# Performance work log

Hardware: AMD Instinct MI355X
Metric: run time of the kernel (lower is better)

## Reference

```python
import jax, jax.numpy as jnp
import numpy as np

D = 128   # latent_dim
H = 128   # mlp_hidden_dim
S = 2     # message_passing_steps
NM = 30000   # mesh nodes
NO = 2000    # obj nodes
EMM = 240000 # mesh->mesh edges
EMO = 60000  # mesh->obj edges


def _ln(h, g, b):
    m = jnp.mean(h, axis=-1, keepdims=True)
    v = jnp.mean((h - m) ** 2, axis=-1, keepdims=True)
    return (h - m) * jax.lax.rsqrt(v + 1e-5) * g + b


def _mlp_ln(h, W0, b0, W1, b1, W2, b2, g, bt):
    # build_mlp(in, [H]*2, out) + LayerNorm(out)
    h = jax.nn.relu(h @ W0 + b0)
    h = jax.nn.relu(h @ W1 + b1)
    h = h @ W2 + b2
    return _ln(h, g, bt)


def _edge_conv(x_src, x_dst, ei, ea, W0, b0, W1, b1, W2, b2, g, bt):
    # PyG source_to_target: x_j = src gather (ei[0]), x_i = dst gather (ei[1])
    xi = x_dst[ei[1]]
    xj = x_src[ei[0]]
    msg = _mlp_ln(jnp.concatenate([xi, xj, ea], axis=-1), W0, b0, W1, b1, W2, b2, g, bt)
    aggr = jax.ops.segment_sum(msg, ei[1], num_segments=x_dst.shape[0])
    return ea + msg, aggr  # residual on edge attr; aggr is sum of raw messages


def _node_conv(x, aggr, W0, b0, W1, b1, W2, b2, g, bt):
    return x + _mlp_ln(jnp.concatenate([x, aggr], axis=-1), W0, b0, W1, b1, W2, b2, g, bt)


def setup_inputs() -> dict:
    key = jax.random.key(0)
    ks = jax.random.split(key, 16)
    f = jnp.float32
    x_mesh = jax.random.normal(ks[0], (NM, D), f)
    x_obj = jax.random.normal(ks[1], (NO, D), f)
    ea_mm = jax.random.normal(ks[2], (EMM, D), f)
    ea_mo = jax.random.normal(ks[3], (EMO, D), f)
    ei_mm = jnp.stack([jax.random.randint(ks[4], (EMM,), 0, NM),
                       jax.random.randint(ks[5], (EMM,), 0, NM)]).astype(jnp.int32)
    ei_mo = jnp.stack([jax.random.randint(ks[6], (EMO,), 0, NM),
                       jax.random.randint(ks[7], (EMO,), 0, NO)]).astype(jnp.int32)

    def w(k, shape, fan):
        return jax.random.normal(k, shape, f) * (1.0 / np.sqrt(fan))

    # params stacked as [edge_or_node_type(2), step(S), ...]
    eW0 = w(ks[8], (2, S, 3 * D, H), 3 * D); eb0 = jnp.zeros((2, S, H), f)
    eW1 = w(ks[9], (2, S, H, H), H);         eb1 = jnp.zeros((2, S, H), f)
    eW2 = w(ks[10], (2, S, H, D), H);        eb2 = jnp.zeros((2, S, D), f)
    eg = jnp.ones((2, S, D), f);             ebt = jnp.zeros((2, S, D), f)
    nW0 = w(ks[11], (2, S, 2 * D, H), 2 * D); nb0 = jnp.zeros((2, S, H), f)
    nW1 = w(ks[12], (2, S, H, H), H);         nb1 = jnp.zeros((2, S, H), f)
    nW2 = w(ks[13], (2, S, H, D), H);         nb2 = jnp.zeros((2, S, D), f)
    ng = jnp.ones((2, S, D), f);              nbt = jnp.zeros((2, S, D), f)
    return dict(x_mesh=x_mesh, x_obj=x_obj, ei_mm=ei_mm, ei_mo=ei_mo,
                ea_mm=ea_mm, ea_mo=ea_mo,
                eW0=eW0, eb0=eb0, eW1=eW1, eb1=eb1, eW2=eW2, eb2=eb2, eg=eg, ebt=ebt,
                nW0=nW0, nb0=nb0, nW1=nW1, nb1=nb1, nW2=nW2, nb2=nb2, ng=ng, nbt=nbt)


def reference(x_mesh, x_obj, ei_mm, ei_mo, ea_mm, ea_mo,
              eW0, eb0, eW1, eb1, eW2, eb2, eg, ebt,
              nW0, nb0, nW1, nb1, nW2, nb2, ng, nbt):
    for s in range(S):
        ep = lambda t: (eW0[t, s], eb0[t, s], eW1[t, s], eb1[t, s], eW2[t, s], eb2[t, s], eg[t, s], ebt[t, s])
        npar = lambda t: (nW0[t, s], nb0[t, s], nW1[t, s], nb1[t, s], nW2[t, s], nb2[t, s], ng[t, s], nbt[t, s])
        # edge convs use node features at layer input
        ea_mm, agg_mesh = _edge_conv(x_mesh, x_mesh, ei_mm, ea_mm, *ep(0))
        ea_mo, agg_obj = _edge_conv(x_mesh, x_obj, ei_mo, ea_mo, *ep(1))
        x_mesh = _node_conv(x_mesh, agg_mesh, *npar(0))
        x_obj = _node_conv(x_obj, agg_obj, *npar(1))
    return (x_mesh, x_obj)
```

## Files before the change

### kernel.cpp

```cpp
#include <hip/hip_runtime.h>

#define DD 128
#define NMESH 30000
#define NOBJ 2000
#define EMMN 240000
#define EMON 60000
#define NB_MM (EMMN / 128)
#define NB_MO ((EMON + 127) / 128)
#define NB_NM ((NMESH + 127) / 128)
#define NB_NO ((NOBJ + 127) / 128)

typedef unsigned short u16;
typedef short short8 __attribute__((ext_vector_type(8)));
typedef float f32x4 __attribute__((ext_vector_type(4)));
typedef __bf16 bf16x8 __attribute__((ext_vector_type(8)));

union FragCvt { short8 s; bf16x8 b; };

static __device__ __forceinline__ u16 f2bf(float f) {
  union { float f; unsigned u; } v; v.f = f;
  unsigned r = v.u + 0x7FFFu + ((v.u >> 16) & 1u);
  return (u16)(r >> 16);
}
static __device__ __forceinline__ float bf2f(u16 u) {
  union { unsigned u; float f; } v; v.u = ((unsigned)u) << 16; return v.f;
}
static __device__ __forceinline__ int swz256(int row, int b) {
  return row * 256 + (b ^ ((row & 7) << 4));
}
static __device__ __forceinline__ bf16x8 ldsFrag(const u16* s, int row, int kByte) {
  FragCvt u; u.s = *(const short8*)((const char*)s + swz256(row, kByte));
  return u.b;
}

static __device__ __forceinline__ void gload_lds16(const void* g, void* l) {
  __builtin_amdgcn_global_load_lds((const __attribute__((address_space(1))) void*)g,
                                   (__attribute__((address_space(3))) void*)l, 16, 0, 0);
}

static __device__ __forceinline__ void stage_w_async(u16* sW, const u16* W,
                                                     int rowLen, int colOff, int tid) {
  const int w = tid >> 6, lane = tid & 63;
  #pragma unroll
  for (int j = 0; j < 4; ++j) {
    const int base_row = (j * 8 + w) * 4;
    const int row = base_row + (lane >> 4);
    const int chunk = (lane & 15) ^ (row & 7);
    const u16* g = W + (size_t)row * rowLen + colOff + chunk * 8;
    gload_lds16(g, (char*)sW + base_row * 256);
  }
}

static __device__ __forceinline__ void mfma_128k(const u16* sIn, const u16* sW,
                                                 int wr, int wc, int lrow, int lk,
                                                 f32x4 acc[2][4]) {
  #pragma unroll
  for (int kc = 0; kc < 4; ++kc) {
    bf16x8 a0 = ldsFrag(sIn, wr * 32 + lrow, kc * 64 + lk * 16);
    bf16x8 a1 = ldsFrag(sIn, wr * 32 + 16 + lrow, kc * 64 + lk * 16);
    #pragma unroll
    for (int ct = 0; ct < 4; ++ct) {
      bf16x8 b = ldsFrag(sW, wc * 64 + ct * 16 + lrow, kc * 64 + lk * 16);
      acc[0][ct] = __builtin_amdgcn_mfma_f32_16x16x32_bf16(a0, b, acc[0][ct], 0, 0, 0);
      acc[1][ct] = __builtin_amdgcn_mfma_f32_16x16x32_bf16(a1, b, acc[1][ct], 0, 0, 0);
    }
  }
}

static __device__ __forceinline__ void transition_relu(u16* sIn, const float* sBias, int biasOff,
                                                       int wr, int wc, int lrow, int lk,
                                                       f32x4 acc[2][4]) {
  #pragma unroll
  for (int rt = 0; rt < 2; ++rt) {
    #pragma unroll
    for (int ct = 0; ct < 4; ++ct) {
      const int col = wc * 64 + ct * 16 + lrow;
      const float bias = sBias[biasOff + col];
      #pragma unroll
      for (int r = 0; r < 4; ++r) {
        const int orow = wr * 32 + rt * 16 + lk * 4 + r;
        float v = acc[rt][ct][r] + bias;
        v = fmaxf(v, 0.f);
        *(u16*)((char*)sIn + swz256(orow, col * 2)) = f2bf(v);
        acc[rt][ct][r] = 0.f;
      }
    }
  }
}

static __device__ __forceinline__ void ln_to_sIn(u16* sIn, float* sPart, const float* sBias,
                                                 int wr, int wc, int lrow, int lk,
                                                 f32x4 acc[2][4]) {
  float gv[4], bv[4];
  #pragma unroll
  for (int ct = 0; ct < 4; ++ct) {
    const int col = wc * 64 + ct * 16 + lrow;
    gv[ct] = sBias[384 + col];
    bv[ct] = sBias[512 + col];
  }
  float s1[2][4], s2[2][4];
  #pragma unroll
  for (int rt = 0; rt < 2; ++rt) {
    #pragma unroll
    for (int r = 0; r < 4; ++r) {
      float a = 0.f, b = 0.f;
      #pragma unroll
      for (int ct = 0; ct < 4; ++ct) {
        const int col = wc * 64 + ct * 16 + lrow;
        const float v = acc[rt][ct][r] + sBias[256 + col];
        acc[rt][ct][r] = v;
        a += v; b += v * v;
      }
      #pragma unroll
      for (int m = 1; m < 16; m <<= 1) { a += __shfl_xor(a, m); b += __shfl_xor(b, m); }
      s1[rt][r] = a; s2[rt][r] = b;
    }
  }
  if (lrow == 0) {
    #pragma unroll
    for (int rt = 0; rt < 2; ++rt)
      #pragma unroll
      for (int r = 0; r < 4; ++r) {
        const int e = wr * 32 + rt * 16 + lk * 4 + r;
        sPart[(wc * 128 + e) * 2] = s1[rt][r];
        sPart[(wc * 128 + e) * 2 + 1] = s2[rt][r];
      }
  }
  __syncthreads();
  #pragma unroll
  for (int rt = 0; rt < 2; ++rt)
    #pragma unroll
    for (int r = 0; r < 4; ++r) {
      const int e = wr * 32 + rt * 16 + lk * 4 + r;
      const float t1 = s1[rt][r] + sPart[((1 - wc) * 128 + e) * 2];
      const float t2 = s2[rt][r] + sPart[((1 - wc) * 128 + e) * 2 + 1];
      const float m = t1 * (1.f / 128.f);
      const float var = t2 * (1.f / 128.f) - m * m;
      const float rstd = rsqrtf(var + 1e-5f);
      #pragma unroll
      for (int ct = 0; ct < 4; ++ct) {
        const int col = wc * 64 + ct * 16 + lrow;
        const float ln = (acc[rt][ct][r] - m) * rstd * gv[ct] + bv[ct];
        *(u16*)((char*)sIn + swz256(e, col * 2)) = f2bf(ln);
      }
    }
}

static __device__ __forceinline__ void stage_rows_bf(u16* sIn, const u16* src, int row, int seg) {
  #pragma unroll
  for (int j = 0; j < 4; ++j) {
    short8 v = *(const short8*)(src + seg * 32 + j * 8);
    *(short8*)((char*)sIn + swz256(row, seg * 64 + j * 16)) = v;
  }
}
static __device__ __forceinline__ void stage_rows_f32(u16* sIn, const float* src, int row, int seg) {
  #pragma unroll
  for (int j = 0; j < 4; ++j) {
    const int c0 = seg * 32 + j * 8;
    f32x4 f0 = *(const f32x4*)(src + c0);
    f32x4 f1 = *(const f32x4*)(src + c0 + 4);
    short8 v;
    #pragma unroll
    for (int q = 0; q < 4; ++q) { v[q] = (short)f2bf(f0[q]); v[4 + q] = (short)f2bf(f1[q]); }
    *(short8*)((char*)sIn + swz256(row, seg * 64 + j * 16)) = v;
  }
}

static __device__ void edge_body(int bid,
    const u16* xsrc, const u16* xdst, const int* ei, int E,
    const float* ea_f32, u16* ea_bf,
    const u16* W0T, const u16* W1T, const u16* W2T,
    const float* b0, const float* b1, const float* b2,
    const float* gq, const float* btq, u16* msg_out,
    u16* sIn, u16* sW, float* sBias, float* sPart)
{
  const int tid = threadIdx.x;
  const int wave = tid >> 6, lane = tid & 63;
  const int lrow = lane & 15, lk = lane >> 4;
  const int wr = wave >> 1, wc = wave & 1;
  const int e0 = bid * 128;
  const int row = tid >> 2, seg = tid & 3;
  const int eRow = (e0 + row < E) ? (e0 + row) : (E - 1);

  if (tid < 128) {
    sBias[tid] = b0[tid];
    sBias[128 + tid] = b1[tid];
    sBias[256 + tid] = b2[tid];
    sBias[384 + tid] = gq[tid];
    sBias[512 + tid] = btq[tid];
  }

  const f32x4 zero = {0.f, 0.f, 0.f, 0.f};
  f32x4 acc[2][4];
  #pragma unroll
  for (int i = 0; i < 2; ++i)
    #pragma unroll
    for (int j = 0; j < 4; ++j) acc[i][j] = zero;

  stage_w_async(sW, W0T, 384, 0, tid);
  { const int idx = ei[E + eRow]; stage_rows_bf(sIn, xdst + (size_t)idx * DD, row, seg); }
  __syncthreads();
  mfma_128k(sIn, sW, wr, wc, lrow, lk, acc);
  __syncthreads();

  stage_w_async(sW, W0T, 384, 128, tid);
  { const int idx = ei[eRow]; stage_rows_bf(sIn, xsrc + (size_t)idx * DD, row, seg); }
  __syncthreads();
  mfma_128k(sIn, sW, wr, wc, lrow, lk, acc);
  __syncthreads();

  stage_w_async(sW, W0T, 384, 256, tid);
  if (ea_f32) stage_rows_f32(sIn, ea_f32 + (size_t)eRow * DD, row, seg);
  else        stage_rows_bf(sIn, ea_bf + (size_t)eRow * DD, row, seg);
  __syncthreads();
  mfma_128k(sIn, sW, wr, wc, lrow, lk, acc);
  __syncthreads();

  transition_relu(sIn, sBias, 0, wr, wc, lrow, lk, acc);
  stage_w_async(sW, W1T, 128, 0, tid);
  __syncthreads();
  mfma_128k(sIn, sW, wr, wc, lrow, lk, acc);
  __syncthreads();

  transition_relu(sIn, sBias, 128, wr, wc, lrow, lk, acc);
  stage_w_async(sW, W2T, 128, 0, tid);
  __syncthreads();
  mfma_128k(sIn, sW, wr, wc, lrow, lk, acc);
  __syncthreads();

  ln_to_sIn(sIn, sPart, sBias, wr, wc, lrow, lk, acc);
  __syncthreads();

  const int e = e0 + row;
  if (e < E) {
    short8 msgv[4];
    #pragma unroll
    for (int j = 0; j < 4; ++j)
      msgv[j] = *(const short8*)((const char*)sIn + swz256(row, seg * 64 + j * 16));
    u16* msgRow = msg_out + (size_t)e * DD + seg * 32;
    u16* eaRow  = ea_bf + (size_t)e * DD + seg * 32;
    if (ea_f32) {
      const float* er = ea_f32 + (size_t)e * DD + seg * 32;
      #pragma unroll
      for (int j = 0; j < 4; ++j) {
        f32x4 o0 = *(const f32x4*)(er + j * 8);
        f32x4 o1 = *(const f32x4*)(er + j * 8 + 4);
        short8 en;
        #pragma unroll
        for (int q = 0; q < 4; ++q) {
          en[q]     = (short)f2bf(o0[q] + bf2f((u16)msgv[j][q]));
          en[4 + q] = (short)f2bf(o1[q] + bf2f((u16)msgv[j][4 + q]));
        }
        *(short8*)(eaRow + j * 8) = en;
        *(short8*)(msgRow + j * 8) = msgv[j];
      }
    } else {
      #pragma unroll
      for (int j = 0; j < 4; ++j) {
        short8 old = *(const short8*)(eaRow + j * 8);
        short8 en;
        #pragma unroll
        for (int q = 0; q < 8; ++q)
          en[q] = (short)f2bf(bf2f((u16)old[q]) + bf2f((u16)msgv[j][q]));
        *(short8*)(eaRow + j * 8) = en;
        *(short8*)(msgRow + j * 8) = msgv[j];
      }
    }
  }
}

__global__ __launch_bounds__(512, 2) void edge_conv_kernel(
    const u16* __restrict__ xm_bf, const u16* __restrict__ xo_bf,
    const int* __restrict__ ei_mm, const int* __restrict__ ei_mo,
    const float* __restrict__ eaf_mm, const float* __restrict__ eaf_mo,
    u16* __restrict__ eab_mm, u16* __restrict__ eab_mo,
    const u16* __restrict__ W0a, const u16* __restrict__ W1a, const u16* __restrict__ W2a,
    const u16* __restrict__ W0b, const u16* __restrict__ W1b, const u16* __restrict__ W2b,
    const float* __restrict__ b0a, const float* __restrict__ b1a, const float* __restrict__ b2a,
    const float* __restrict__ ga, const float* __restrict__ bta,
    const float* __restrict__ b0b, const float* __restrict__ b1b, const float* __restrict__ b2b,
    const float* __restrict__ gb, const float* __restrict__ btb,
    u16* __restrict__ msg_mm, u16* __restrict__ msg_mo)
{
  __shared__ u16 sIn[128 * 128];
  __shared__ u16 sW[128 * 128];
  __shared__ float sBias[5 * 128];
  __shared__ float sPart[2 * 128 * 2];
  if ((int)blockIdx.x < NB_MM)
    edge_body(blockIdx.x, xm_bf, xm_bf, ei_mm, EMMN, eaf_mm, eab_mm,
              W0a, W1a, W2a, b0a, b1a, b2a, ga, bta, msg_mm, sIn, sW, sBias, sPart);
  else
    edge_body(blockIdx.x - NB_MM, xm_bf, xo_bf, ei_mo, EMON, eaf_mo, eab_mo,
              W0b, W1b, W2b, b0b, b1b, b2b, gb, btb, msg_mo, sIn, sW, sBias, sPart);
}

static __device__ void node_body(int bid, u16* x_bf, const float* aggin, float* x_f32, int N,
    const u16* W0T, const u16* W1T, const u16* W2T,
    const float* b0, const float* b1, const float* b2,
    const float* gq, const float* btq,
    u16* sIn, u16* sW, float* sBias, float* sPart)
{
  const int tid = threadIdx.x;
  const int wave = tid >> 6, lane = tid & 63;
  const int lrow = lane & 15, lk = lane >> 4;
  const int wr = wave >> 1, wc = wave & 1;
  const int n0 = bid * 128;
  const int row = tid >> 2, seg = tid & 3;
  const int nRow = (n0 + row < N) ? (n0 + row) : (N - 1);

  if (tid < 128) {
    sBias[tid] = b0[tid];
    sBias[128 + tid] = b1[tid];
    sBias[256 + tid] = b2[tid];
    sBias[384 + tid] = gq[tid];
    sBias[512 + tid] = btq[tid];
  }

  const f32x4 zero = {0.f, 0.f, 0.f, 0.f};
  f32x4 acc[2][4];
  #pragma unroll
  for (int i = 0; i < 2; ++i)
    #pragma unroll
    for (int j = 0; j < 4; ++j) acc[i][j] = zero;

  stage_w_async(sW, W0T, 256, 0, tid);
  stage_rows_bf(sIn, x_bf + (size_t)nRow * DD, row, seg);
  __syncthreads();
  mfma_128k(sIn, sW, wr, wc, lrow, lk, acc);
  __syncthreads();

  stage_w_async(sW, W0T, 256, 128, tid);
  stage_rows_f32(sIn, aggin + (size_t)nRow * DD, row, seg);
  __syncthreads();
  mfma_128k(sIn, sW, wr, wc, lrow, lk, acc);
  __syncthreads();

  transition_relu(sIn, sBias, 0, wr, wc, lrow, lk, acc);
  stage_w_async(sW, W1T, 128, 0, tid);
  __syncthreads();
  mfma_128k(sIn, sW, wr, wc, lrow, lk, acc);
  __syncthreads();

  transition_relu(sIn, sBias, 128, wr, wc, lrow, lk, acc);
  stage_w_async(sW, W2T, 128, 0, tid);
  __syncthreads();
  mfma_128k(sIn, sW, wr, wc, lrow, lk, acc);
  __syncthreads();

  ln_to_sIn(sIn, sPart, sBias, wr, wc, lrow, lk, acc);
  __syncthreads();

  const int n = n0 + row;
  if (n < N) {
    short8 lnv[4];
    #pragma unroll
    for (int j = 0; j < 4; ++j)
      lnv[j] = *(const short8*)((const char*)sIn + swz256(row, seg * 64 + j * 16));
    float* xr = x_f32 + (size_t)n * DD + seg * 32;
    u16* xb = x_bf + (size_t)n * DD + seg * 32;
    #pragma unroll
    for (int j = 0; j < 4; ++j) {
      f32x4 o0 = *(const f32x4*)(xr + j * 8);
      f32x4 o1 = *(const f32x4*)(xr + j * 8 + 4);
      f32x4 n0v, n1v;
      short8 pb;
      #pragma unroll
      for (int q = 0; q < 4; ++q) {
        n0v[q] = o0[q] + bf2f((u16)lnv[j][q]);
        n1v[q] = o1[q] + bf2f((u16)lnv[j][4 + q]);
        pb[q]     = (short)f2bf(n0v[q]);
        pb[4 + q] = (short)f2bf(n1v[q]);
      }
      *(f32x4*)(xr + j * 8) = n0v;
      *(f32x4*)(xr + j * 8 + 4) = n1v;
      *(short8*)(xb + j * 8) = pb;
    }
  }
}

__global__ __launch_bounds__(512, 2) void node_conv_kernel(
    u16* __restrict__ xm_bf, u16* __restrict__ xo_bf,
    const float* __restrict__ agg_m, const float* __restrict__ agg_o,
    float* __restrict__ xf_m, float* __restrict__ xf_o,
    const u16* __restrict__ W0a, const u16* __restrict__ W1a, const u16* __restrict__ W2a,
    const u16* __restrict__ W0b, const u16* __restrict__ W1b, const u16* __restrict__ W2b,
    const float* __restrict__ b0a, const float* __restrict__ b1a, const float* __restrict__ b2a,
    const float* __restrict__ ga, const float* __restrict__ bta,
    const float* __restrict__ b0b, const float* __restrict__ b1b, const float* __restrict__ b2b,
    const float* __restrict__ gb, const float* __restrict__ btb)
{
  __shared__ u16 sIn[128 * 128];
  __shared__ u16 sW[128 * 128];
  __shared__ float sBias[5 * 128];
  __shared__ float sPart[2 * 128 * 2];
  if ((int)blockIdx.x < NB_NM)
    node_body(blockIdx.x, xm_bf, agg_m, xf_m, NMESH,
              W0a, W1a, W2a, b0a, b1a, b2a, ga, bta, sIn, sW, sBias, sPart);
  else
    node_body(blockIdx.x - NB_NM, xo_bf, agg_o, xf_o, NOBJ,
              W0b, W1b, W2b, b0b, b1b, b2b, gb, btb, sIn, sW, sBias, sPart);
}

__global__ void hist_kernel(const int* __restrict__ ei_mm, const int* __restrict__ ei_mo,
                            int* __restrict__ deg_m, int* __restrict__ deg_o) {
  int i = blockIdx.x * blockDim.x + threadIdx.x;
  if (i < EMMN) atomicAdd(&deg_m[ei_mm[EMMN + i]], 1);
  else { int j = i - EMMN; if (j < EMON) atomicAdd(&deg_o[ei_mo[EMON + j]], 1); }
}

__global__ __launch_bounds__(1024) void scan_kernel(
    const int* __restrict__ deg_m, int* __restrict__ start_m, int* __restrict__ cur_m,
    const int* __restrict__ deg_o, int* __restrict__ start_o, int* __restrict__ cur_o) {
  const int* deg; int* start; int* cursor; int N;
  if (blockIdx.x == 0) { deg = deg_m; start = start_m; cursor = cur_m; N = NMESH; }
  else                 { deg = deg_o; start = start_o; cursor = cur_o; N = NOBJ; }
  __shared__ int lds[1024];
  const int t = threadIdx.x;
  const int chunk = (N + 1023) >> 10;
  const int base = t * chunk;
  const int end = min(base + chunk, N);
  int s = 0;
  for (int i = base; i < end; ++i) s += deg[i];
  lds[t] = s;
  __syncthreads();
  for (int d = 1; d < 1024; d <<= 1) {
    int v = (t >= d) ? lds[t - d] : 0;
    __syncthreads();
    lds[t] += v;
    __syncthreads();
  }
  int off = lds[t] - s;
  for (int i = base; i < end; ++i) { start[i] = off; cursor[i] = off; off += deg[i]; }
  if (t == 1023) start[N] = lds[1023];
}

__global__ void scatter_kernel(const int* __restrict__ ei_mm, const int* __restrict__ ei_mo,
                               int* __restrict__ cur_m, int* __restrict__ cur_o,
                               int* __restrict__ perm_m, int* __restrict__ perm_o) {
  int i = blockIdx.x * blockDim.x + threadIdx.x;
  if (i < EMMN) { int p = atomicAdd(&cur_m[ei_mm[EMMN + i]], 1); perm_m[p] = i; }
  else { int j = i - EMMN; if (j < EMON) { int p = atomicAdd(&cur_o[ei_mo[EMON + j]], 1); perm_o[p] = j; } }
}

__global__ __launch_bounds__(256) void agg_gather_kernel(
    const u16* __restrict__ msg_m, const int* __restrict__ start_m, const int* __restrict__ perm_m,
    float* __restrict__ agg_m,
    const u16* __restrict__ msg_o, const int* __restrict__ start_o, const int* __restrict__ perm_o,
    float* __restrict__ agg_o)
{
  const int wave = threadIdx.x >> 6, lane = threadIdx.x & 63;
  int idx = blockIdx.x * 4 + wave;
  const u16* msg; const int* start; const int* perm; float* agg; int n;
  if (idx < NMESH) { msg = msg_m; start = start_m; perm = perm_m; agg = agg_m; n = idx; }
  else {
    n = idx - NMESH;
    if (n >= NOBJ) return;
    msg = msg_o; start = start_o; perm = perm_o; agg = agg_o;
  }
  const int i0 = start[n], i1 = start[n + 1];
  float a0 = 0.f, a1 = 0.f;
  int i = i0;
  for (; i + 1 < i1; i += 2) {
    const int e1 = perm[i], e2 = perm[i + 1];
    unsigned v1 = *(const unsigned*)(msg + (size_t)e1 * DD + lane * 2);
    unsigned v2 = *(const unsigned*)(msg + (size_t)e2 * DD + lane * 2);
    a0 += bf2f((u16)(v1 & 0xFFFFu)) + bf2f((u16)(v2 & 0xFFFFu));
    a1 += bf2f((u16)(v1 >> 16)) + bf2f((u16)(v2 >> 16));
  }
  if (i < i1) {
    const int e1 = perm[i];
    unsigned v1 = *(const unsigned*)(msg + (size_t)e1 * DD + lane * 2);
    a0 += bf2f((u16)(v1 & 0xFFFFu));
    a1 += bf2f((u16)(v1 >> 16));
  }
  float* ar = agg + (size_t)n * DD + lane * 2;
  ar[0] = a0;
  ar[1] = a1;
}

static __device__ __forceinline__ void wcvt(const float* src, u16* dst, int K, int b, int t) {
  int i = b * 256 + t;
  int n = i & 127;
  int k = (i >> 7) % K;
  int sl = i / (K * 128);
  dst[((size_t)sl * 128 + n) * K + k] = f2bf(src[i]);
}

__global__ void prep_kernel(
    const float* __restrict__ eW0, const float* __restrict__ eW1, const float* __restrict__ eW2,
    const float* __restrict__ nW0, const float* __restrict__ nW1, const float* __restrict__ nW2,
    u16* __restrict__ eW0T, u16* __restrict__ eW1T, u16* __restrict__ eW2T,
    u16* __restrict__ nW0T, u16* __restrict__ nW1T, u16* __restrict__ nW2T,
    int* __restrict__ deg_m, int* __restrict__ deg_o,
    const float* __restrict__ xm, const float* __restrict__ xo,
    float* __restrict__ xf, u16* __restrict__ xmb, u16* __restrict__ xob)
{
  const int b = blockIdx.x, t = threadIdx.x;
  if (b < 768)        wcvt(eW0, eW0T, 384, b, t);
  else if (b < 1024)  wcvt(eW1, eW1T, 128, b - 768, t);
  else if (b < 1280)  wcvt(eW2, eW2T, 128, b - 1024, t);
  else if (b < 1792)  wcvt(nW0, nW0T, 256, b - 1280, t);
  else if (b < 2048)  wcvt(nW1, nW1T, 128, b - 1792, t);
  else if (b < 2304)  wcvt(nW2, nW2T, 128, b - 2048, t);
  else if (b < 2429) {
    int i = (b - 2304) * 256 + t;
    if (i < NMESH) deg_m[i] = 0;
    else if (i < NMESH + NOBJ) deg_o[i - NMESH] = 0;
  } else {
    int i = (b - 2429) * 256 + t;
    const int tm = NMESH * DD;
    if (i < tm) { float v = xm[i]; xf[i] = v; xmb[i] = f2bf(v); }
    else { int j = i - tm; float v = xo[j]; xf[tm + j] = v; xob[j] = f2bf(v); }
  }
}

extern "C" void kernel_launch(void* const* d_in, const int* in_sizes, int n_in,
                              void* d_out, int out_size, void* d_ws, size_t ws_size,
                              hipStream_t stream)
{
  const float* x_mesh = (const float*)d_in[0];
  const float* x_obj  = (const float*)d_in[1];
  const int*   ei_mm  = (const int*)d_in[2];
  const int*   ei_mo  = (const int*)d_in[3];
  const float* ea_mm  = (const float*)d_in[4];
  const float* ea_mo  = (const float*)d_in[5];
  const float* eW0 = (const float*)d_in[6];
  const float* eb0 = (const float*)d_in[7];
  const float* eW1 = (const float*)d_in[8];
  const float* eb1 = (const float*)d_in[9];
  const float* eW2 = (const float*)d_in[10];
  const float* eb2 = (const float*)d_in[11];
  const float* eg  = (const float*)d_in[12];
  const float* ebt = (const float*)d_in[13];
  const float* nW0 = (const float*)d_in[14];
  const float* nb0 = (const float*)d_in[15];
  const float* nW1 = (const float*)d_in[16];
  const float* nb1 = (const float*)d_in[17];
  const float* nW2 = (const float*)d_in[18];
  const float* nb2 = (const float*)d_in[19];
  const float* ng  = (const float*)d_in[20];
  const float* nbt = (const float*)d_in[21];

  u16* eamm_bf = (u16*)d_ws;
  u16* eamo_bf = eamm_bf + (size_t)EMMN * DD;
  u16* xm_bf   = eamo_bf + (size_t)EMON * DD;
  u16* xo_bf   = xm_bf + (size_t)NMESH * DD;
  float* agg_m = (float*)(xo_bf + (size_t)NOBJ * DD);
  float* agg_o = agg_m + (size_t)NMESH * DD;
  u16* eW0T = (u16*)(agg_o + (size_t)NOBJ * DD);
  u16* eW1T = eW0T + (size_t)4 * 128 * 384;
  u16* eW2T = eW1T + (size_t)4 * 128 * 128;
  u16* nW0T = eW2T + (size_t)4 * 128 * 128;
  u16* nW1T = nW0T + (size_t)4 * 128 * 256;
  u16* nW2T = nW1T + (size_t)4 * 128 * 128;
  u16* msg_mm = nW2T + (size_t)4 * 128 * 128;
  u16* msg_mo = msg_mm + (size_t)EMMN * DD;
  int* deg_m   = (int*)(msg_mo + (size_t)EMON * DD);
  int* start_m = deg_m + NMESH;
  int* cur_m   = start_m + NMESH + 1;
  int* perm_mm = cur_m + NMESH;
  int* deg_o   = perm_mm + EMMN;
  int* start_o = deg_o + NOBJ;
  int* cur_o   = start_o + NOBJ + 1;
  int* perm_mo = cur_o + NOBJ;

  float* xf_m = (float*)d_out;
  float* xf_o = xf_m + (size_t)NMESH * DD;

  prep_kernel<<<18429, 256, 0, stream>>>(eW0, eW1, eW2, nW0, nW1, nW2,
                                         eW0T, eW1T, eW2T, nW0T, nW1T, nW2T,
                                         deg_m, deg_o, x_mesh, x_obj, xf_m, xm_bf, xo_bf);
  hist_kernel<<<(EMMN + EMON + 255) / 256, 256, 0, stream>>>(ei_mm, ei_mo, deg_m, deg_o);
  scan_kernel<<<2, 1024, 0, stream>>>(deg_m, start_m, cur_m, deg_o, start_o, cur_o);
  scatter_kernel<<<(EMMN + EMON + 255) / 256, 256, 0, stream>>>(ei_mm, ei_mo, cur_m, cur_o,
                                                                perm_mm, perm_mo);

  for (int s = 0; s < 2; ++s) {
    const int sa = 0 * 2 + s, sb = 1 * 2 + s;
    edge_conv_kernel<<<NB_MM + NB_MO, 512, 0, stream>>>(
        xm_bf, xo_bf, ei_mm, ei_mo,
        (s == 0) ? ea_mm : (const float*)nullptr,
        (s == 0) ? ea_mo : (const float*)nullptr,
        eamm_bf, eamo_bf,
        eW0T + (size_t)sa * 128 * 384, eW1T + (size_t)sa * 128 * 128, eW2T + (size_t)sa * 128 * 128,
        eW0T + (size_t)sb * 128 * 384, eW1T + (size_t)sb * 128 * 128, eW2T + (size_t)sb * 128 * 128,
        eb0 + sa * 128, eb1 + sa * 128, eb2 + sa * 128, eg + sa * 128, ebt + sa * 128,
        eb0 + sb * 128, eb1 + sb * 128, eb2 + sb * 128, eg + sb * 128, ebt + sb * 128,
        msg_mm, msg_mo);
    agg_gather_kernel<<<(NMESH + NOBJ + 3) / 4, 256, 0, stream>>>(
        msg_mm, start_m, perm_mm, agg_m, msg_mo, start_o, perm_mo, agg_o);
    node_conv_kernel<<<NB_NM + NB_NO, 512, 0, stream>>>(
        xm_bf, xo_bf, agg_m, agg_o, xf_m, xf_o,
        nW0T + (size_t)sa * 128 * 256, nW1T + (size_t)sa * 128 * 128, nW2T + (size_t)sa * 128 * 128,
        nW0T + (size_t)sb * 128 * 256, nW1T + (size_t)sb * 128 * 128, nW2T + (size_t)sb * 128 * 128,
        nb0 + sa * 128, nb1 + sa * 128, nb2 + sa * 128, ng + sa * 128, nbt + sa * 128,
        nb0 + sb * 128, nb1 + sb * 128, nb2 + sb * 128, ng + sb * 128, nbt + sb * 128);
  }
}
```

Before: 745.9 us.

## Halve row tiles and register-prefetch next weight and input stages

Edge and node MLP kernels now process 64 rows per block with 256 threads instead of 128 rows with 512. The async global-to-LDS weight staging is replaced by register double-buffering: the next weight slice and input rows are loaded into registers while the current MFMA stage runs, then written to LDS after the barrier. The residual input (edge attr or node features) is also prefetched before the LayerNorm epilogue. The aim is to hide global load latency and raise occupancy, at the cost of extra registers and re-staging the full weight matrices for twice as many blocks.

Result: slower. 1.015 ms (+36.1%).

```diff
diff --git a/kernel.cpp b/kernel.cpp
--- a/kernel.cpp
+++ b/kernel.cpp
@@ -5,10 +5,10 @@
 #define NOBJ 2000
 #define EMMN 240000
 #define EMON 60000
-#define NB_MM (EMMN / 128)
-#define NB_MO ((EMON + 127) / 128)
-#define NB_NM ((NMESH + 127) / 128)
-#define NB_NO ((NOBJ + 127) / 128)
+#define NB_MM (EMMN / 64)
+#define NB_MO ((EMON + 63) / 64)
+#define NB_NM ((NMESH + 63) / 64)
+#define NB_NO ((NOBJ + 63) / 64)
 
 typedef unsigned short u16;
 typedef short short8 __attribute__((ext_vector_type(8)));
@@ -33,21 +33,37 @@
   return u.b;
 }
 
-static __device__ __forceinline__ void gload_lds16(const void* g, void* l) {
-  __builtin_amdgcn_global_load_lds((const __attribute__((address_space(1))) void*)g,
-                                   (__attribute__((address_space(3))) void*)l, 16, 0, 0);
-}
-
-static __device__ __forceinline__ void stage_w_async(u16* sW, const u16* W,
-                                                     int rowLen, int colOff, int tid) {
-  const int w = tid >> 6, lane = tid & 63;
+static __device__ __forceinline__ void ld_w(short8 w[8], const u16* W, int rowLen,
+                                            int colOff, int wrow, int wh) {
+  const u16* g = W + (size_t)wrow * rowLen + colOff + wh * 64;
+  #pragma unroll
+  for (int j = 0; j < 8; ++j) w[j] = *(const short8*)(g + j * 8);
+}
+static __device__ __forceinline__ void wr_w(u16* sW, const short8 w[8], int wrow, int wh) {
+  #pragma unroll
+  for (int j = 0; j < 8; ++j)
+    *(short8*)((char*)sW + swz256(wrow, wh * 128 + j * 16)) = w[j];
+}
+static __device__ __forceinline__ void ld_rows_bf(short8 a[4], const u16* src, int seg) {
+  #pragma unroll
+  for (int j = 0; j < 4; ++j) a[j] = *(const short8*)(src + seg * 32 + j * 8);
+}
+static __device__ __forceinline__ void wr_rows(u16* sIn, const short8 a[4], int row, int seg) {
+  #pragma unroll
+  for (int j = 0; j < 4; ++j)
+    *(short8*)((char*)sIn + swz256(row, seg * 64 + j * 16)) = a[j];
+}
+static __device__ __forceinline__ void ld_rows_f32(f32x4 ef[8], const float* src, int seg) {
+  #pragma unroll
+  for (int j = 0; j < 8; ++j) ef[j] = *(const f32x4*)(src + seg * 32 + j * 4);
+}
+static __device__ __forceinline__ void wr_rows_f32(u16* sIn, const f32x4 ef[8], int row, int seg) {
   #pragma unroll
   for (int j = 0; j < 4; ++j) {
-    const int base_row = (j * 8 + w) * 4;
-    const int row = base_row + (lane >> 4);
-    const int chunk = (lane & 15) ^ (row & 7);
-    const u16* g = W + (size_t)row * rowLen + colOff + chunk * 8;
-    gload_lds16(g, (char*)sW + base_row * 256);
+    short8 v;
+    #pragma unroll
+    for (int q = 0; q < 4; ++q) { v[q] = (short)f2bf(ef[2*j][q]); v[4+q] = (short)f2bf(ef[2*j+1][q]); }
+    *(short8*)((char*)sIn + swz256(row, seg * 64 + j * 16)) = v;
   }
 }
 
@@ -122,8 +138,8 @@
       #pragma unroll
       for (int r = 0; r < 4; ++r) {
         const int e = wr * 32 + rt * 16 + lk * 4 + r;
-        sPart[(wc * 128 + e) * 2] = s1[rt][r];
-        sPart[(wc * 128 + e) * 2 + 1] = s2[rt][r];
+        sPart[(wc * 64 + e) * 2] = s1[rt][r];
+        sPart[(wc * 64 + e) * 2 + 1] = s2[rt][r];
       }
   }
   __syncthreads();
@@ -132,8 +148,8 @@
     #pragma unroll
     for (int r = 0; r < 4; ++r) {
       const int e = wr * 32 + rt * 16 + lk * 4 + r;
-      const float t1 = s1[rt][r] + sPart[((1 - wc) * 128 + e) * 2];
-      const float t2 = s2[rt][r] + sPart[((1 - wc) * 128 + e) * 2 + 1];
+      const float t1 = s1[rt][r] + sPart[((1 - wc) * 64 + e) * 2];
+      const float t2 = s2[rt][r] + sPart[((1 - wc) * 64 + e) * 2 + 1];
       const float m = t1 * (1.f / 128.f);
       const float var = t2 * (1.f / 128.f) - m * m;
       const float rstd = rsqrtf(var + 1e-5f);
@@ -144,26 +160,6 @@
         *(u16*)((char*)sIn + swz256(e, col * 2)) = f2bf(ln);
       }
     }
-}
-
-static __device__ __forceinline__ void stage_rows_bf(u16* sIn, const u16* src, int row, int seg) {
-  #pragma unroll
-  for (int j = 0; j < 4; ++j) {
-    short8 v = *(const short8*)(src + seg * 32 + j * 8);
-    *(short8*)((char*)sIn + swz256(row, seg * 64 + j * 16)) = v;
-  }
-}
-static __device__ __forceinline__ void stage_rows_f32(u16* sIn, const float* src, int row, int seg) {
-  #pragma unroll
-  for (int j = 0; j < 4; ++j) {
-    const int c0 = seg * 32 + j * 8;
-    f32x4 f0 = *(const f32x4*)(src + c0);
-    f32x4 f1 = *(const f32x4*)(src + c0 + 4);
-    short8 v;
-    #pragma unroll
-    for (int q = 0; q < 4; ++q) { v[q] = (short)f2bf(f0[q]); v[4 + q] = (short)f2bf(f1[q]); }
-    *(short8*)((char*)sIn + swz256(row, seg * 64 + j * 16)) = v;
-  }
 }
 
 static __device__ void edge_body(int bid,
@@ -178,9 +174,11 @@
   const int wave = tid >> 6, lane = tid & 63;
   const int lrow = lane & 15, lk = lane >> 4;
   const int wr = wave >> 1, wc = wave & 1;
-  const int e0 = bid * 128;
+  const int e0 = bid * 64;
   const int row = tid >> 2, seg = tid & 3;
   const int eRow = (e0 + row < E) ? (e0 + row) : (E - 1);
+  const int wrow = tid >> 1, wh = tid & 1;
+  const bool eaf = (ea_f32 != nullptr);
 
   if (tid < 128) {
     sBias[tid] = b0[tid];
@@ -197,36 +195,51 @@
     #pragma unroll
     for (int j = 0; j < 4; ++j) acc[i][j] = zero;
 
-  stage_w_async(sW, W0T, 384, 0, tid);
-  { const int idx = ei[E + eRow]; stage_rows_bf(sIn, xdst + (size_t)idx * DD, row, seg); }
-  __syncthreads();
-  mfma_128k(sIn, sW, wr, wc, lrow, lk, acc);
-  __syncthreads();
-
-  stage_w_async(sW, W0T, 384, 128, tid);
-  { const int idx = ei[eRow]; stage_rows_bf(sIn, xsrc + (size_t)idx * DD, row, seg); }
-  __syncthreads();
-  mfma_128k(sIn, sW, wr, wc, lrow, lk, acc);
-  __syncthreads();
-
-  stage_w_async(sW, W0T, 384, 256, tid);
-  if (ea_f32) stage_rows_f32(sIn, ea_f32 + (size_t)eRow * DD, row, seg);
-  else        stage_rows_bf(sIn, ea_bf + (size_t)eRow * DD, row, seg);
+  short8 w[8], a[4];
+  f32x4 ef[8];
+
+  ld_w(w, W0T, 384, 0, wrow, wh);
+  { const int idx = ei[E + eRow]; ld_rows_bf(a, xdst + (size_t)idx * DD, seg); }
+  wr_w(sW, w, wrow, wh);
+  wr_rows(sIn, a, row, seg);
+  ld_w(w, W0T, 384, 128, wrow, wh);
+  { const int idx = ei[eRow]; ld_rows_bf(a, xsrc + (size_t)idx * DD, seg); }
+  __syncthreads();
+  mfma_128k(sIn, sW, wr, wc, lrow, lk, acc);
+  __syncthreads();
+
+  wr_w(sW, w, wrow, wh);
+  wr_rows(sIn, a, row, seg);
+  ld_w(w, W0T, 384, 256, wrow, wh);
+  if (eaf) ld_rows_f32(ef, ea_f32 + (size_t)eRow * DD, seg);
+  else     ld_rows_bf(a, ea_bf + (size_t)eRow * DD, seg);
+  __syncthreads();
+  mfma_128k(sIn, sW, wr, wc, lrow, lk, acc);
+  __syncthreads();
+
+  wr_w(sW, w, wrow, wh);
+  if (eaf) wr_rows_f32(sIn, ef, row, seg);
+  else     wr_rows(sIn, a, row, seg);
+  ld_w(w, W1T, 128, 0, wrow, wh);
   __syncthreads();
   mfma_128k(sIn, sW, wr, wc, lrow, lk, acc);
   __syncthreads();
 
   transition_relu(sIn, sBias, 0, wr, wc, lrow, lk, acc);
-  stage_w_async(sW, W1T, 128, 0, tid);
+  wr_w(sW, w, wrow, wh);
+  ld_w(w, W2T, 128, 0, wrow, wh);
   __syncthreads();
   mfma_128k(sIn, sW, wr, wc, lrow, lk, acc);
   __syncthreads();
 
   transition_relu(sIn, sBias, 128, wr, wc, lrow, lk, acc);
-  stage_w_async(sW, W2T, 128, 0, tid);
-  __syncthreads();
-  mfma_128k(sIn, sW, wr, wc, lrow, lk, acc);
-  __syncthreads();
+  wr_w(sW, w, wrow, wh);
+  __syncthreads();
+  mfma_128k(sIn, sW, wr, wc, lrow, lk, acc);
+  __syncthreads();
+
+  if (eaf) ld_rows_f32(ef, ea_f32 + (size_t)eRow * DD, seg);
+  else     ld_rows_bf(a, ea_bf + (size_t)eRow * DD, seg);
 
   ln_to_sIn(sIn, sPart, sBias, wr, wc, lrow, lk, acc);
   __syncthreads();
@@ -239,37 +252,27 @@
       msgv[j] = *(const short8*)((const char*)sIn + swz256(row, seg * 64 + j * 16));
     u16* msgRow = msg_out + (size_t)e * DD + seg * 32;
     u16* eaRow  = ea_bf + (size_t)e * DD + seg * 32;
-    if (ea_f32) {
-      const float* er = ea_f32 + (size_t)e * DD + seg * 32;
-      #pragma unroll
-      for (int j = 0; j < 4; ++j) {
-        f32x4 o0 = *(const f32x4*)(er + j * 8);
-        f32x4 o1 = *(const f32x4*)(er + j * 8 + 4);
-        short8 en;
+    #pragma unroll
+    for (int j = 0; j < 4; ++j) {
+      short8 en;
+      if (eaf) {
         #pragma unroll
         for (int q = 0; q < 4; ++q) {
-          en[q]     = (short)f2bf(o0[q] + bf2f((u16)msgv[j][q]));
-          en[4 + q] = (short)f2bf(o1[q] + bf2f((u16)msgv[j][4 + q]));
+          en[q]     = (short)f2bf(ef[2*j][q]   + bf2f((u16)msgv[j][q]));
+          en[4 + q] = (short)f2bf(ef[2*j+1][q] + bf2f((u16)msgv[j][4 + q]));
         }
-        *(short8*)(eaRow + j * 8) = en;
-        *(short8*)(msgRow + j * 8) = msgv[j];
-      }
-    } else {
-      #pragma unroll
-      for (int j = 0; j < 4; ++j) {
-        short8 old = *(const short8*)(eaRow + j * 8);
-        short8 en;
+      } else {
         #pragma unroll
         for (int q = 0; q < 8; ++q)
-          en[q] = (short)f2bf(bf2f((u16)old[q]) + bf2f((u16)msgv[j][q]));
-        *(short8*)(eaRow + j * 8) = en;
-        *(short8*)(msgRow + j * 8) = msgv[j];
+          en[q] = (short)f2bf(bf2f((u16)a[j][q]) + bf2f((u16)msgv[j][q]));
       }
+      *(short8*)(eaRow + j * 8) = en;
+      *(short8*)(msgRow + j * 8) = msgv[j];
     }
   }
 }
 
-__global__ __launch_bounds__(512, 2) void edge_conv_kernel(
+__global__ __launch_bounds__(256, 3) void edge_conv_kernel(
     const u16* __restrict__ xm_bf, const u16* __restrict__ xo_bf,
     const int* __restrict__ ei_mm, const int* __restrict__ ei_mo,
     const float* __restrict__ eaf_mm, const float* __restrict__ eaf_mo,
@@ -282,10 +285,10 @@
     const float* __restrict__ gb, const float* __restrict__ btb,
     u16* __restrict__ msg_mm, u16* __restrict__ msg_mo)
 {
-  __shared__ u16 sIn[128 * 128];
+  __shared__ u16 sIn[64 * 128];
   __shared__ u16 sW[128 * 128];
   __shared__ float sBias[5 * 128];
-  __shared__ float sPart[2 * 128 * 2];
+  __shared__ float sPart[2 * 64 * 2];
   if ((int)blockIdx.x < NB_MM)
     edge_body(blockIdx.x, xm_bf, xm_bf, ei_mm, EMMN, eaf_mm, eab_mm,
               W0a, W1a, W2a, b0a, b1a, b2a, ga, bta, msg_mm, sIn, sW, sBias, sPart);
@@ -304,9 +307,10 @@
   const int wave = tid >> 6, lane = tid & 63;
   const int lrow = lane & 15, lk = lane >> 4;
   const int wr = wave >> 1, wc = wave & 1;
-  const int n0 = bid * 128;
+  const int n0 = bid * 64;
   const int row = tid >> 2, seg = tid & 3;
   const int nRow = (n0 + row < N) ? (n0 + row) : (N - 1);
+  const int wrow = tid >> 1, wh = tid & 1;
 
   if (tid < 128) {
     sBias[tid] = b0[tid];
@@ -323,29 +327,40 @@
     #pragma unroll
     for (int j = 0; j < 4; ++j) acc[i][j] = zero;
 
-  stage_w_async(sW, W0T, 256, 0, tid);
-  stage_rows_bf(sIn, x_bf + (size_t)nRow * DD, row, seg);
-  __syncthreads();
-  mfma_128k(sIn, sW, wr, wc, lrow, lk, acc);
-  __syncthreads();
-
-  stage_w_async(sW, W0T, 256, 128, tid);
-  stage_rows_f32(sIn, aggin + (size_t)nRow * DD, row, seg);
+  short8 w[8], a[4];
+  f32x4 ef[8];
+
+  ld_w(w, W0T, 256, 0, wrow, wh);
+  ld_rows_bf(a, x_bf + (size_t)nRow * DD, seg);
+  wr_w(sW, w, wrow, wh);
+  wr_rows(sIn, a, row, seg);
+  ld_w(w, W0T, 256, 128, wrow, wh);
+  ld_rows_f32(ef, aggin + (size_t)nRow * DD, seg);
+  __syncthreads();
+  mfma_128k(sIn, sW, wr, wc, lrow, lk, acc);
+  __syncthreads();
+
+  wr_w(sW, w, wrow, wh);
+  wr_rows_f32(sIn, ef, row, seg);
+  ld_w(w, W1T, 128, 0, wrow, wh);
   __syncthreads();
   mfma_128k(sIn, sW, wr, wc, lrow, lk, acc);
   __syncthreads();
 
   transition_relu(sIn, sBias, 0, wr, wc, lrow, lk, acc);
-  stage_w_async(sW, W1T, 128, 0, tid);
+  wr_w(sW, w, wrow, wh);
+  ld_w(w, W2T, 128, 0, wrow, wh);
   __syncthreads();
   mfma_128k(sIn, sW, wr, wc, lrow, lk, acc);
   __syncthreads();
 
   transition_relu(sIn, sBias, 128, wr, wc, lrow, lk, acc);
-  stage_w_async(sW, W2T, 128, 0, tid);
-  __syncthreads();
-  mfma_128k(sIn, sW, wr, wc, lrow, lk, acc);
-  __syncthreads();
+  wr_w(sW, w, wrow, wh);
+  __syncthreads();
+  mfma_128k(sIn, sW, wr, wc, lrow, lk, acc);
+  __syncthreads();
+
+  ld_rows_f32(ef, x_f32 + (size_t)nRow * DD, seg);
 
   ln_to_sIn(sIn, sPart, sBias, wr, wc, lrow, lk, acc);
   __syncthreads();
@@ -360,14 +375,12 @@
     u16* xb = x_bf + (size_t)n * DD + seg * 32;
     #pragma unroll
     for (int j = 0; j < 4; ++j) {
-      f32x4 o0 = *(const f32x4*)(xr + j * 8);
-      f32x4 o1 = *(const f32x4*)(xr + j * 8 + 4);
       f32x4 n0v, n1v;
       short8 pb;
       #pragma unroll
       for (int q = 0; q < 4; ++q) {
-        n0v[q] = o0[q] + bf2f((u16)lnv[j][q]);
-        n1v[q] = o1[q] + bf2f((u16)lnv[j][4 + q]);
+        n0v[q] = ef[2*j][q]   + bf2f((u16)lnv[j][q]);
+        n1v[q] = ef[2*j+1][q] + bf2f((u16)lnv[j][4 + q]);
         pb[q]     = (short)f2bf(n0v[q]);
         pb[4 + q] = (short)f2bf(n1v[q]);
       }
@@ -378,7 +391,7 @@
   }
 }
 
-__global__ __launch_bounds__(512, 2) void node_conv_kernel(
+__global__ __launch_bounds__(256, 3) void node_conv_kernel(
     u16* __restrict__ xm_bf, u16* __restrict__ xo_bf,
     const float* __restrict__ agg_m, const float* __restrict__ agg_o,
     float* __restrict__ xf_m, float* __restrict__ xf_o,
@@ -389,10 +402,10 @@
     const float* __restrict__ b0b, const float* __restrict__ b1b, const float* __restrict__ b2b,
     const float* __restrict__ gb, const float* __restrict__ btb)
 {
-  __shared__ u16 sIn[128 * 128];
+  __shared__ u16 sIn[64 * 128];
   __shared__ u16 sW[128 * 128];
   __shared__ float sBias[5 * 128];
-  __shared__ float sPart[2 * 128 * 2];
+  __shared__ float sPart[2 * 64 * 2];
   if ((int)blockIdx.x < NB_NM)
     node_body(blockIdx.x, xm_bf, agg_m, xf_m, NMESH,
               W0a, W1a, W2a, b0a, b1a, b2a, ga, bta, sIn, sW, sBias, sPart);
@@ -577,7 +590,7 @@
 
   for (int s = 0; s < 2; ++s) {
     const int sa = 0 * 2 + s, sb = 1 * 2 + s;
-    edge_conv_kernel<<<NB_MM + NB_MO, 512, 0, stream>>>(
+    edge_conv_kernel<<<NB_MM + NB_MO, 256, 0, stream>>>(
         xm_bf, xo_bf, ei_mm, ei_mo,
         (s == 0) ? ea_mm : (const float*)nullptr,
         (s == 0) ? ea_mo : (const float*)nullptr,
@@ -589,7 +602,7 @@
         msg_mm, msg_mo);
     agg_gather_kernel<<<(NMESH + NOBJ + 3) / 4, 256, 0, stream>>>(
         msg_mm, start_m, perm_mm, agg_m, msg_mo, start_o, perm_mo, agg_o);
-    node_conv_kernel<<<NB_NM + NB_NO, 512, 0, stream>>>(
+    node_conv_kernel<<<NB_NM + NB_NO, 256, 0, stream>>>(
         xm_bf, xo_bf, agg_m, agg_o, xf_m, xf_o,
         nW0T + (size_t)sa * 128 * 256, nW1T + (size_t)sa * 128 * 128, nW2T + (size_t)sa * 128 * 128,
         nW0T + (size_t)sb * 128 * 256, nW1T + (size_t)sb * 128 * 128, nW2T + (size_t)sb * 128 * 128,
```
